# Kernel optimization log

Measured on AMD Instinct MI355X. Metric: run time of the kernel, lower is better.

## Reference

```python
import jax, jax.numpy as jnp
import numpy as np

# dims matching init_kwargs
B, T, F = 512, 2048, 32
BULK, COH = 8, 8
OUT = 6
COH_SIZE, BULK_SIZE = COH * 2, BULK * 3

# Turon cohesive-law constants (bilinear traction-separation)
D0, DF = 0.01, 0.1          # onset / final effective opening
# J2 plasticity constants (plane-stress, linear isotropic hardening)
E_MOD, NU = 1000.0, 0.3
SIGY0, HARD = 10.0, 100.0
G_MOD = E_MOD / (2.0 * (1.0 + NU))
_c = E_MOD / (1.0 - NU ** 2)
D_NP = np.array([[_c, _c * NU, 0.0], [_c * NU, _c, 0.0], [0.0, 0.0, _c * (1.0 - NU) / 2.0]], dtype=np.float32)
DINV_NP = np.linalg.inv(D_NP).astype(np.float32)


def setup_inputs() -> dict:
    key = jax.random.key(0)
    k1, k2, k3, k4 = jax.random.split(key, 4)
    x = jax.random.normal(k1, (B, T, F), jnp.float32) * 0.05
    W11 = jax.random.normal(k2, (COH_SIZE, F), jnp.float32) / np.sqrt(F)
    W12 = jax.random.normal(k3, (BULK_SIZE, F), jnp.float32) / np.sqrt(F)
    W2 = jax.random.normal(k4, (OUT, BULK_SIZE), jnp.float32) / np.sqrt(BULK_SIZE)
    return {"x": x, "W11": W11, "W12": W12, "W2": W2}


def _forward(x, W11, W12, W2):
    Bb, Tt, _ = x.shape
    # tiny per-point linear layers, batched over (B, T) up front
    coh_in = jnp.einsum('btf,cf->btc', x, W11).reshape(Bb, Tt, COH, 2)    # separations
    bulk_in = jnp.einsum('btf,cf->btc', x, W12).reshape(Bb, Tt, BULK, 3)  # strains
    W2s = jax.nn.softplus(W2)  # softLayer: positivity-constrained weights
    D = jnp.asarray(D_NP)
    DINV = jnp.asarray(DINV_NP)

    def step(carry, inp):
        d_hist, eps_p, kappa = carry          # [B,COH], [B,BULK,3], [B,BULK]
        delta, eps = inp                      # [B,COH,2], [B,BULK,3]
        # --- Turon cohesive update: history = max damage; loading flag ---
        dn, ds = delta[..., 0], delta[..., 1]
        lam = jnp.sqrt(jnp.maximum(dn, 0.0) ** 2 + ds ** 2 + 1e-12)
        d_new = jnp.clip(DF * (lam - D0) / (lam * (DF - D0)), 0.0, 1.0)
        d = jnp.maximum(d_hist, d_new)
        loading = (d_new > d_hist).astype(eps.dtype)
        # (cohesive tractions are computed in the torch code but never consumed)
        # --- J2 plane-stress return mapping with linear hardening ---
        sig_tr = jnp.einsum('bpi,ji->bpj', eps - eps_p, D)
        sxx, syy, sxy = sig_tr[..., 0], sig_tr[..., 1], sig_tr[..., 2]
        seq = jnp.sqrt(sxx ** 2 - sxx * syy + syy ** 2 + 3.0 * sxy ** 2 + 1e-12)
        sigY = SIGY0 + HARD * kappa
        dk = jnp.maximum(seq - sigY, 0.0) / (3.0 * G_MOD + HARD)
        f = jnp.where(seq > sigY, (sigY + HARD * dk) / seq, 1.0)
        sig = f[..., None] * sig_tr
        eps_p_n = eps - jnp.einsum('bpj,ij->bpi', sig, DINV)
        kappa_n = kappa + dk
        # --- damage coupling: if not loading, degrade bulk stress by (1-d) ---
        dam_b = d[:, :BULK]
        load_b = loading[:, :BULK]
        sig = jnp.where((load_b == 0.0)[..., None], sig * (1.0 - dam_b)[..., None], sig)
        out_t = sig.reshape(Bb, BULK_SIZE) @ W2s.T  # [B,OUT]
        return (d, eps_p_n, kappa_n), out_t

    carry0 = (jnp.zeros((Bb, COH), x.dtype), jnp.zeros((Bb, BULK, 3), x.dtype), jnp.zeros((Bb, BULK), x.dtype))
    _, outs = jax.lax.scan(step, carry0, (coh_in.swapaxes(0, 1), bulk_in.swapaxes(0, 1)))
    return outs.swapaxes(0, 1)  # [B,T,OUT]


def reference(x, W11, W12, W2):
    return _forward(x, W11, W12, W2)
```

## Files before the change

kernel.cpp:

```cpp
#include <hip/hip_runtime.h>
#include <math.h>

static constexpr int BT  = 512;
static constexpr int TT  = 2048;

static constexpr float C00 = (float)(1000.0 / (1.0 - 0.09));
static constexpr float C01 = (float)((1000.0 / (1.0 - 0.09)) * 0.3);
static constexpr float C22 = (float)((1000.0 / (1.0 - 0.09)) * 0.35);
static constexpr float INV3GH = (float)(1.0 / (3.0 * (1000.0 / 2.6) + 100.0));
static constexpr float SQ3 = 1.7320508075688772f;
static constexpr float IR3 = 0.57735026918962576f;

typedef float f2 __attribute__((ext_vector_type(2)));

__device__ __forceinline__ float softplus_f(float v) {
    return fmaxf(v, 0.0f) + log1pf(expf(-fabsf(v)));
}

__global__ __launch_bounds__(512) void k_fused(
    const float* __restrict__ x, const float* __restrict__ W11,
    const float* __restrict__ W12, const float* __restrict__ W2,
    float* __restrict__ out)
{
    __shared__ __align__(16) float w11s[16 * 36];
    __shared__ __align__(16) float w12d[24 * 36];
    __shared__ float w2s[144];
    __shared__ __align__(16) float xs[2][64 * 36];
    __shared__ float red[2][64 * 51];

    const int tid  = threadIdx.x;
    const int lane = tid & 63;
    const int wv   = tid >> 6;
    const int b    = blockIdx.x;

    if (tid < 512) w11s[(tid >> 5) * 36 + (tid & 31)] = W11[tid];
    if (tid < 256) {
        int i = tid + 512;
        w11s[(i >> 5) * 36 + (i & 31)] = W11[i];
    }
    for (int i = tid; i < 768; i += 512) {
        int r = i >> 5, fc = i & 31;
        int p = r / 3, j = r - p * 3;
        const float* wb = W12 + p * 96 + fc;
        float v;
        if (j == 0)      v = C00 * wb[0]  + C01 * wb[32];
        else if (j == 1) v = C01 * wb[0]  + C00 * wb[32];
        else             v = (C22 * wb[64]) * SQ3;
        w12d[r * 36 + fc] = v;
    }
    if (tid < 144) {
        float v = softplus_f(W2[tid]);
        if ((tid % 24) % 3 == 2) v *= IR3;
        w2s[tid] = v;
    }
    const float4* xg4 = (const float4*)x + (size_t)b * (TT * 8);
    {
        float4 val = xg4[tid];
        int t = tid >> 3, c = tid & 7;
        *(float4*)&xs[0][t * 36 + 4 * c] = val;
    }
    __syncthreads();

    float w2r0[6], w2r1[6], w2r2[6];
    #pragma unroll
    for (int k = 0; k < 6; ++k) {
        w2r0[k] = w2s[k * 24 + 3 * wv];
        w2r1[k] = w2s[k * 24 + 3 * wv + 1];
        w2r2[k] = w2s[k * 24 + 3 * wv + 2];
    }
    const float4* wa0 = (const float4*)(w11s + (2 * wv) * 36);
    const float4* wa1 = (const float4*)(w11s + (2 * wv + 1) * 36);
    const float4* wb0 = (const float4*)(w12d + (3 * wv) * 36);
    const float4* wb1 = (const float4*)(w12d + (3 * wv + 1) * 36);
    const float4* wb2 = (const float4*)(w12d + (3 * wv + 2) * 36);

    float Pxx = 0.f, Pyy = 0.f, Pxy = 0.f;
    float sigY = 10.f, sigY2 = 100.f, d0 = 0.f;

    for (int w = 0; w < 32; ++w) {
        float4 nval;
        const bool have = (w < 31);
        if (have) nval = xg4[(w + 1) * 512 + tid];

        const float* xr = &xs[w & 1][lane * 36];
        f2 dn2 = {0.f, 0.f}, ds2 = {0.f, 0.f};
        f2 e02 = {0.f, 0.f}, e12 = {0.f, 0.f}, e22 = {0.f, 0.f};
        #pragma unroll
        for (int c = 0; c < 8; ++c) {
            float4 xf = *(const float4*)(xr + 4 * c);
            float4 a0 = wa0[c], a1 = wa1[c];
            float4 b0 = wb0[c], b1 = wb1[c], b2 = wb2[c];
            f2 xlo = {xf.x, xf.y}, xhi = {xf.z, xf.w};
            f2 t0, t1;
            t0 = (f2){a0.x, a0.y}; t1 = (f2){a0.z, a0.w};
            dn2 = xlo * t0 + dn2;  dn2 = xhi * t1 + dn2;
            t0 = (f2){a1.x, a1.y}; t1 = (f2){a1.z, a1.w};
            ds2 = xlo * t0 + ds2;  ds2 = xhi * t1 + ds2;
            t0 = (f2){b0.x, b0.y}; t1 = (f2){b0.z, b0.w};
            e02 = xlo * t0 + e02;  e02 = xhi * t1 + e02;
            t0 = (f2){b1.x, b1.y}; t1 = (f2){b1.z, b1.w};
            e12 = xlo * t0 + e12;  e12 = xhi * t1 + e12;
            t0 = (f2){b2.x, b2.y}; t1 = (f2){b2.z, b2.w};
            e22 = xlo * t0 + e22;  e22 = xhi * t1 + e22;
        }
        float dn = dn2.x + dn2.y, ds = ds2.x + ds2.y;
        float e0 = e02.x + e02.y, e1 = e12.x + e12.y, e2 = e22.x + e22.y;

        float dnp  = fmaxf(dn, 0.f);
        float lam  = sqrtf(fmaf(dnp, dnp, fmaf(ds, ds, 1e-12f)));
        float dnew = (0.1f * (lam - 0.01f)) / (lam * 0.09f);
        dnew = fminf(fmaxf(dnew, 0.f), 1.f);

        float sxx = e0 - Pxx, syy = e1 - Pyy, sxy = e2 - Pxy;
        float q = fmaf(sxy, sxy, 1e-12f);
        q = fmaf(syy, syy, q);
        q = fmaf(sxx, sxx - syy, q);
        float f = 1.0f;

        unsigned long long mask = __ballot(q > sigY2);
        while (mask) {
            int ts = __ffsll((long long)mask) - 1;
            float qs  = __shfl(q, ts);
            float sxs = __shfl(sxx, ts);
            float sys = __shfl(syy, ts);
            float sps = __shfl(sxy, ts);
            float rq  = __builtin_amdgcn_rsqf(qs);
            float seq = qs * rq;
            float dk  = (seq - sigY) * INV3GH;
            float fn  = fmaf(100.f, dk, sigY);
            float fs  = fn * rq;
            float om  = 1.0f - fs;
            Pxx = fmaf(om, sxs, Pxx);
            Pyy = fmaf(om, sys, Pyy);
            Pxy = fmaf(om, sps, Pxy);
            sigY = fn; sigY2 = fn * fn;
            if (lane == ts) f = fs;
            bool redo = lane > ts;
            if (redo) {
                sxx = e0 - Pxx; syy = e1 - Pyy; sxy = e2 - Pxy;
                q = fmaf(sxy, sxy, 1e-12f);
                q = fmaf(syy, syy, q);
                q = fmaf(sxx, sxx - syy, q);
            }
            mask = __ballot(redo && (q > sigY2));
        }

        float m = dnew;
        #pragma unroll
        for (int off = 1; off < 64; off <<= 1) {
            float t2 = __shfl_up(m, off);
            if (lane >= off) m = fmaxf(m, t2);
        }
        float de = __shfl_up(m, 1);
        de = (lane == 0) ? d0 : fmaxf(d0, de);
        bool loading = dnew > de;
        float di = fmaxf(de, dnew);
        d0 = fmaxf(d0, __shfl(m, 63));

        float scale = loading ? f : f * (1.0f - di);
        float o0 = scale * sxx, o1 = scale * syy, o2 = scale * sxy;

        #pragma unroll
        for (int k = 0; k < 6; ++k) {
            float cpk = fmaf(o0, w2r0[k], fmaf(o1, w2r1[k], o2 * w2r2[k]));
            red[w & 1][lane * 51 + k * 8 + wv] = cpk;
        }

        if (w > 0 && tid < 384) {
            int t = tid & 63, k = tid >> 6;
            const float* rp = &red[(w - 1) & 1][t * 51 + k * 8];
            float acc = ((rp[0] + rp[1]) + (rp[2] + rp[3]))
                      + ((rp[4] + rp[5]) + (rp[6] + rp[7]));
            out[((size_t)b * TT + (w - 1) * 64 + t) * 6 + k] = acc;
        }

        if (have) {
            int t = tid >> 3, c = tid & 7;
            *(float4*)&xs[(w + 1) & 1][t * 36 + 4 * c] = nval;
        }
        __syncthreads();
    }

    if (tid < 384) {
        int t = tid & 63, k = tid >> 6;
        const float* rp = &red[1][t * 51 + k * 8];
        float acc = ((rp[0] + rp[1]) + (rp[2] + rp[3]))
                  + ((rp[4] + rp[5]) + (rp[6] + rp[7]));
        out[((size_t)b * TT + 31 * 64 + t) * 6 + k] = acc;
    }
}

extern "C" void kernel_launch(void* const* d_in, const int* in_sizes, int n_in,
                              void* d_out, int out_size, void* d_ws, size_t ws_size,
                              hipStream_t stream)
{
    const float* x   = (const float*)d_in[0];
    const float* W11 = (const float*)d_in[1];
    const float* W12 = (const float*)d_in[2];
    const float* W2  = (const float*)d_in[3];
    float* out = (float*)d_out;

    hipLaunchKernelGGL(k_fused, dim3(BT), dim3(512), 0, stream,
                       x, W11, W12, W2, out);
}
```

Before: 143.5 us.

## Process two 64-step time windows per loop iteration with quad-buffered x staging

```diff
diff --git a/kernel.cpp b/kernel.cpp
--- a/kernel.cpp
+++ b/kernel.cpp
@@ -15,6 +15,45 @@
 
 __device__ __forceinline__ float softplus_f(float v) {
     return fmaxf(v, 0.0f) + log1pf(expf(-fabsf(v)));
+}
+
+__device__ __forceinline__ void plastic_window(
+    float e0, float e1, float e2, int lane,
+    float& Pxx, float& Pyy, float& Pxy, float& sigY, float& sigY2,
+    float& sxx, float& syy, float& sxy, float& f)
+{
+    sxx = e0 - Pxx; syy = e1 - Pyy; sxy = e2 - Pxy;
+    float q = fmaf(sxy, sxy, 1e-12f);
+    q = fmaf(syy, syy, q);
+    q = fmaf(sxx, sxx - syy, q);
+    f = 1.0f;
+    unsigned long long mask = __ballot(q > sigY2);
+    while (mask) {
+        int ts = __ffsll((long long)mask) - 1;
+        float qs  = __shfl(q, ts);
+        float sxs = __shfl(sxx, ts);
+        float sys = __shfl(syy, ts);
+        float sps = __shfl(sxy, ts);
+        float rq  = __builtin_amdgcn_rsqf(qs);
+        float seq = qs * rq;
+        float dk  = (seq - sigY) * INV3GH;
+        float fn  = fmaf(100.f, dk, sigY);
+        float fs  = fn * rq;
+        float om  = 1.0f - fs;
+        Pxx = fmaf(om, sxs, Pxx);
+        Pyy = fmaf(om, sys, Pyy);
+        Pxy = fmaf(om, sps, Pxy);
+        sigY = fn; sigY2 = fn * fn;
+        if (lane == ts) f = fs;
+        bool redo = lane > ts;
+        if (redo) {
+            sxx = e0 - Pxx; syy = e1 - Pyy; sxy = e2 - Pxy;
+            q = fmaf(sxy, sxy, 1e-12f);
+            q = fmaf(syy, syy, q);
+            q = fmaf(sxx, sxx - syy, q);
+        }
+        mask = __ballot(redo && (q > sigY2));
+    }
 }
 
 __global__ __launch_bounds__(512) void k_fused(
@@ -25,7 +64,7 @@
     __shared__ __align__(16) float w11s[16 * 36];
     __shared__ __align__(16) float w12d[24 * 36];
     __shared__ float w2s[144];
-    __shared__ __align__(16) float xs[2][64 * 36];
+    __shared__ __align__(16) float xs[4][64 * 36];
     __shared__ float red[2][64 * 51];
 
     const int tid  = threadIdx.x;
@@ -55,9 +94,11 @@
     }
     const float4* xg4 = (const float4*)x + (size_t)b * (TT * 8);
     {
-        float4 val = xg4[tid];
         int t = tid >> 3, c = tid & 7;
-        *(float4*)&xs[0][t * 36 + 4 * c] = val;
+        float4 v0 = xg4[tid];
+        float4 v1 = xg4[512 + tid];
+        *(float4*)&xs[0][t * 36 + 4 * c] = v0;
+        *(float4*)&xs[1][t * 36 + 4 * c] = v1;
     }
     __syncthreads();
 
@@ -77,116 +118,114 @@
     float Pxx = 0.f, Pyy = 0.f, Pxy = 0.f;
     float sigY = 10.f, sigY2 = 100.f, d0 = 0.f;
 
-    for (int w = 0; w < 32; ++w) {
-        float4 nval;
-        const bool have = (w < 31);
-        if (have) nval = xg4[(w + 1) * 512 + tid];
-
-        const float* xr = &xs[w & 1][lane * 36];
-        f2 dn2 = {0.f, 0.f}, ds2 = {0.f, 0.f};
-        f2 e02 = {0.f, 0.f}, e12 = {0.f, 0.f}, e22 = {0.f, 0.f};
+    for (int s = 0; s < 16; ++s) {
+        const int w0 = 2 * s, w1 = w0 + 1;
+        const bool have = (s < 15);
+        float4 nv0, nv1;
+        if (have) {
+            nv0 = xg4[(w0 + 2) * 512 + tid];
+            nv1 = xg4[(w1 + 2) * 512 + tid];
+        }
+
+        const float* xr0 = &xs[w0 & 3][lane * 36];
+        const float* xr1 = &xs[w1 & 3][lane * 36];
+        f2 dnA = {0,0}, dsA = {0,0}, e0A = {0,0}, e1A = {0,0}, e2A = {0,0};
+        f2 dnB = {0,0}, dsB = {0,0}, e0B = {0,0}, e1B = {0,0}, e2B = {0,0};
         #pragma unroll
         for (int c = 0; c < 8; ++c) {
-            float4 xf = *(const float4*)(xr + 4 * c);
             float4 a0 = wa0[c], a1 = wa1[c];
             float4 b0 = wb0[c], b1 = wb1[c], b2 = wb2[c];
-            f2 xlo = {xf.x, xf.y}, xhi = {xf.z, xf.w};
+            float4 xf0 = *(const float4*)(xr0 + 4 * c);
+            float4 xf1 = *(const float4*)(xr1 + 4 * c);
+            f2 xlo0 = {xf0.x, xf0.y}, xhi0 = {xf0.z, xf0.w};
+            f2 xlo1 = {xf1.x, xf1.y}, xhi1 = {xf1.z, xf1.w};
             f2 t0, t1;
             t0 = (f2){a0.x, a0.y}; t1 = (f2){a0.z, a0.w};
-            dn2 = xlo * t0 + dn2;  dn2 = xhi * t1 + dn2;
+            dnA = xlo0 * t0 + dnA;  dnA = xhi0 * t1 + dnA;
+            dnB = xlo1 * t0 + dnB;  dnB = xhi1 * t1 + dnB;
             t0 = (f2){a1.x, a1.y}; t1 = (f2){a1.z, a1.w};
-            ds2 = xlo * t0 + ds2;  ds2 = xhi * t1 + ds2;
+            dsA = xlo0 * t0 + dsA;  dsA = xhi0 * t1 + dsA;
+            dsB = xlo1 * t0 + dsB;  dsB = xhi1 * t1 + dsB;
             t0 = (f2){b0.x, b0.y}; t1 = (f2){b0.z, b0.w};
-            e02 = xlo * t0 + e02;  e02 = xhi * t1 + e02;
+            e0A = xlo0 * t0 + e0A;  e0A = xhi0 * t1 + e0A;
+            e0B = xlo1 * t0 + e0B;  e0B = xhi1 * t1 + e0B;
             t0 = (f2){b1.x, b1.y}; t1 = (f2){b1.z, b1.w};
-            e12 = xlo * t0 + e12;  e12 = xhi * t1 + e12;
+            e1A = xlo0 * t0 + e1A;  e1A = xhi0 * t1 + e1A;
+            e1B = xlo1 * t0 + e1B;  e1B = xhi1 * t1 + e1B;
             t0 = (f2){b2.x, b2.y}; t1 = (f2){b2.z, b2.w};
-            e22 = xlo * t0 + e22;  e22 = xhi * t1 + e22;
-        }
-        float dn = dn2.x + dn2.y, ds = ds2.x + ds2.y;
-        float e0 = e02.x + e02.y, e1 = e12.x + e12.y, e2 = e22.x + e22.y;
-
-        float dnp  = fmaxf(dn, 0.f);
-        float lam  = sqrtf(fmaf(dnp, dnp, fmaf(ds, ds, 1e-12f)));
-        float dnew = (0.1f * (lam - 0.01f)) / (lam * 0.09f);
-        dnew = fminf(fmaxf(dnew, 0.f), 1.f);
-
-        float sxx = e0 - Pxx, syy = e1 - Pyy, sxy = e2 - Pxy;
-        float q = fmaf(sxy, sxy, 1e-12f);
-        q = fmaf(syy, syy, q);
-        q = fmaf(sxx, sxx - syy, q);
-        float f = 1.0f;
-
-        unsigned long long mask = __ballot(q > sigY2);
-        while (mask) {
-            int ts = __ffsll((long long)mask) - 1;
-            float qs  = __shfl(q, ts);
-            float sxs = __shfl(sxx, ts);
-            float sys = __shfl(syy, ts);
-            float sps = __shfl(sxy, ts);
-            float rq  = __builtin_amdgcn_rsqf(qs);
-            float seq = qs * rq;
-            float dk  = (seq - sigY) * INV3GH;
-            float fn  = fmaf(100.f, dk, sigY);
-            float fs  = fn * rq;
-            float om  = 1.0f - fs;
-            Pxx = fmaf(om, sxs, Pxx);
-            Pyy = fmaf(om, sys, Pyy);
-            Pxy = fmaf(om, sps, Pxy);
-            sigY = fn; sigY2 = fn * fn;
-            if (lane == ts) f = fs;
-            bool redo = lane > ts;
-            if (redo) {
-                sxx = e0 - Pxx; syy = e1 - Pyy; sxy = e2 - Pxy;
-                q = fmaf(sxy, sxy, 1e-12f);
-                q = fmaf(syy, syy, q);
-                q = fmaf(sxx, sxx - syy, q);
-            }
-            mask = __ballot(redo && (q > sigY2));
-        }
-
-        float m = dnew;
+            e2A = xlo0 * t0 + e2A;  e2A = xhi0 * t1 + e2A;
+            e2B = xlo1 * t0 + e2B;  e2B = xhi1 * t1 + e2B;
+        }
+        float dn0 = dnA.x + dnA.y, ds0 = dsA.x + dsA.y;
+        float e00 = e0A.x + e0A.y, e10 = e1A.x + e1A.y, e20 = e2A.x + e2A.y;
+        float dn1 = dnB.x + dnB.y, ds1 = dsB.x + dsB.y;
+        float e01 = e0B.x + e0B.y, e11 = e1B.x + e1B.y, e21 = e2B.x + e2B.y;
+
+        float dnp0  = fmaxf(dn0, 0.f);
+        float lam0  = sqrtf(fmaf(dnp0, dnp0, fmaf(ds0, ds0, 1e-12f)));
+        float dnew0 = (0.1f * (lam0 - 0.01f)) / (lam0 * 0.09f);
+        dnew0 = fminf(fmaxf(dnew0, 0.f), 1.f);
+        float dnp1  = fmaxf(dn1, 0.f);
+        float lam1  = sqrtf(fmaf(dnp1, dnp1, fmaf(ds1, ds1, 1e-12f)));
+        float dnew1 = (0.1f * (lam1 - 0.01f)) / (lam1 * 0.09f);
+        dnew1 = fminf(fmaxf(dnew1, 0.f), 1.f);
+
+        float m0 = dnew0, m1 = dnew1;
         #pragma unroll
         for (int off = 1; off < 64; off <<= 1) {
-            float t2 = __shfl_up(m, off);
-            if (lane >= off) m = fmaxf(m, t2);
-        }
-        float de = __shfl_up(m, 1);
-        de = (lane == 0) ? d0 : fmaxf(d0, de);
-        bool loading = dnew > de;
-        float di = fmaxf(de, dnew);
-        d0 = fmaxf(d0, __shfl(m, 63));
-
-        float scale = loading ? f : f * (1.0f - di);
-        float o0 = scale * sxx, o1 = scale * syy, o2 = scale * sxy;
+            float t0 = __shfl_up(m0, off);
+            float t1 = __shfl_up(m1, off);
+            if (lane >= off) { m0 = fmaxf(m0, t0); m1 = fmaxf(m1, t1); }
+        }
+        float de0 = __shfl_up(m0, 1);
+        de0 = (lane == 0) ? d0 : fmaxf(d0, de0);
+        bool loading0 = dnew0 > de0;
+        float di0 = fmaxf(de0, dnew0);
+        float d0a = fmaxf(d0, __shfl(m0, 63));
+        float de1 = __shfl_up(m1, 1);
+        de1 = (lane == 0) ? d0a : fmaxf(d0a, de1);
+        bool loading1 = dnew1 > de1;
+        float di1 = fmaxf(de1, dnew1);
+        d0 = fmaxf(d0a, __shfl(m1, 63));
+
+        float sxx0, syy0, sxy0, f0;
+        plastic_window(e00, e10, e20, lane, Pxx, Pyy, Pxy, sigY, sigY2,
+                       sxx0, syy0, sxy0, f0);
+        float scale0 = loading0 ? f0 : f0 * (1.0f - di0);
+        float o00 = scale0 * sxx0, o10 = scale0 * syy0, o20 = scale0 * sxy0;
+
+        float sxx1, syy1, sxy1, f1;
+        plastic_window(e01, e11, e21, lane, Pxx, Pyy, Pxy, sigY, sigY2,
+                       sxx1, syy1, sxy1, f1);
+        float scale1 = loading1 ? f1 : f1 * (1.0f - di1);
+        float o01 = scale1 * sxx1, o11 = scale1 * syy1, o21 = scale1 * sxy1;
 
         #pragma unroll
         for (int k = 0; k < 6; ++k) {
-            float cpk = fmaf(o0, w2r0[k], fmaf(o1, w2r1[k], o2 * w2r2[k]));
-            red[w & 1][lane * 51 + k * 8 + wv] = cpk;
-        }
-
-        if (w > 0 && tid < 384) {
+            float c0 = fmaf(o00, w2r0[k], fmaf(o10, w2r1[k], o20 * w2r2[k]));
+            float c1 = fmaf(o01, w2r0[k], fmaf(o11, w2r1[k], o21 * w2r2[k]));
+            red[0][lane * 51 + k * 8 + wv] = c0;
+            red[1][lane * 51 + k * 8 + wv] = c1;
+        }
+        __syncthreads();
+
+        if (tid < 384) {
             int t = tid & 63, k = tid >> 6;
-            const float* rp = &red[(w - 1) & 1][t * 51 + k * 8];
-            float acc = ((rp[0] + rp[1]) + (rp[2] + rp[3]))
-                      + ((rp[4] + rp[5]) + (rp[6] + rp[7]));
-            out[((size_t)b * TT + (w - 1) * 64 + t) * 6 + k] = acc;
-        }
-
+            const float* rp0 = &red[0][t * 51 + k * 8];
+            float a0 = ((rp0[0] + rp0[1]) + (rp0[2] + rp0[3]))
+                     + ((rp0[4] + rp0[5]) + (rp0[6] + rp0[7]));
+            out[((size_t)b * TT + w0 * 64 + t) * 6 + k] = a0;
+            const float* rp1 = &red[1][t * 51 + k * 8];
+            float a1 = ((rp1[0] + rp1[1]) + (rp1[2] + rp1[3]))
+                     + ((rp1[4] + rp1[5]) + (rp1[6] + rp1[7]));
+            out[((size_t)b * TT + w1 * 64 + t) * 6 + k] = a1;
+        }
         if (have) {
             int t = tid >> 3, c = tid & 7;
-            *(float4*)&xs[(w + 1) & 1][t * 36 + 4 * c] = nval;
+            *(float4*)&xs[(w0 + 2) & 3][t * 36 + 4 * c] = nv0;
+            *(float4*)&xs[(w1 + 2) & 3][t * 36 + 4 * c] = nv1;
         }
         __syncthreads();
-    }
-
-    if (tid < 384) {
-        int t = tid & 63, k = tid >> 6;
-        const float* rp = &red[1][t * 51 + k * 8];
-        float acc = ((rp[0] + rp[1]) + (rp[2] + rp[3]))
-                  + ((rp[4] + rp[5]) + (rp[6] + rp[7]));
-        out[((size_t)b * TT + 31 * 64 + t) * 6 + k] = acc;
     }
 }
 
```

After: 119.8 us. 16.5% less time.
